# Optimization experiments

Measured on AMD Instinct MI355X. Metric: run time of the kernel, lower is better.

The kernel has to match this reference:

```python
import jax, jax.numpy as jnp
import numpy as np

N = 8192   # collocation points
H = 64     # hidden_dim (d_out of each KANLayer)
UH = 8     # unary_hidden_dim


def setup_inputs() -> dict:
    key = jax.random.key(0)
    ks = jax.random.split(key, 16)
    d = {}
    d["x"] = jax.random.normal(ks[0], (N, 1), dtype=jnp.float32)
    d["t"] = jax.random.normal(ks[1], (N, 1), dtype=jnp.float32)
    dims = [(2, H), (H, H), (H, H)]  # (d_in, d_out) per KANLayer
    idx = 2
    for l, (di, do) in enumerate(dims):
        d[f"W1_{l}"] = jax.random.normal(ks[idx], (do, di, UH), dtype=jnp.float32) * 0.5; idx += 1
        d[f"B1_{l}"] = jax.random.normal(ks[idx], (do, di, UH), dtype=jnp.float32) * 0.1; idx += 1
        d[f"W2_{l}"] = jax.random.normal(ks[idx], (do, di, UH), dtype=jnp.float32) * 0.5; idx += 1
        d[f"B2_{l}"] = jax.random.normal(ks[idx], (do, di), dtype=jnp.float32) * 0.1; idx += 1
    d["W_out"] = jax.random.normal(ks[14], (1, H), dtype=jnp.float32) * 0.1
    d["b_out"] = jnp.zeros((1,), dtype=jnp.float32)
    return d


def kan_layer(h, W1, B1, W2, B2):
    """Stacked KANLayer: y[n,j] = sum_i ( W2[j,i,:] . tanh(h[n,i]*W1[j,i,:] + B1[j,i,:]) + B2[j,i] ).
    h: (N, d_in); W1,B1,W2: (d_out, d_in, UH); B2: (d_out, d_in). Returns (N, d_out)."""
    hid = jnp.tanh(h[:, None, :, None] * W1[None] + B1[None])  # (N, d_out, d_in, UH)
    return jnp.einsum('ndih,dih->nd', hid, W2) + B2.sum(axis=1)


def reference(x, t, W1_0, B1_0, W2_0, B2_0, W1_1, B1_1, W2_1, B2_1,
              W1_2, B1_2, W2_2, B2_2, W_out, b_out):
    h = jnp.concatenate([x, t], axis=1)  # (N, 2)
    layers = [(W1_0, B1_0, W2_0, B2_0),
              (W1_1, B1_1, W2_1, B2_1),
              (W1_2, B1_2, W2_2, B2_2)]
    for W1, B1, W2, B2 in layers:
        h = jnp.tanh(kan_layer(h, W1, B1, W2, B2))
    u = h @ W_out.T + b_out  # (N, 1)
    return u
```

## Files before the change

kernel.cpp:

```cpp
#include <hip/hip_runtime.h>
#include <math.h>


#define C2L 2.88539008177792681472f
#define P_CHEB 20
#define M_SAMP 32

__device__ __forceinline__ float tanh_hw(float z) {
  float e = __builtin_amdgcn_exp2f(z * C2L);
  float r = __builtin_amdgcn_rcpf(1.0f + e);
  return fmaf(r, -2.0f, 1.0f);
}

__global__ __launch_bounds__(256) void kan_prep(
    const float* __restrict__ W1_1, const float* __restrict__ B1_1,
    const float* __restrict__ W2_1, const float* __restrict__ B2_1,
    const float* __restrict__ W1_2, const float* __restrict__ B1_2,
    const float* __restrict__ W2_2, const float* __restrict__ B2_2,
    float* __restrict__ G1, float* __restrict__ G2)
{
  const int g = blockIdx.x * 256 + threadIdx.x;
  const int k = g & 7;
  const int ji = (g >> 3) & 4095;
  const int layer = g >> 15;
  const float* __restrict__ W1 = layer ? W1_2 : W1_1;
  const float* __restrict__ B1 = layer ? B1_2 : B1_1;
  const float* __restrict__ W2 = layer ? W2_2 : W2_1;
  const float* __restrict__ B2 = layer ? B2_2 : B2_1;
  float* __restrict__ G = layer ? G2 : G1;

  const float w  = W1[ji * 8 + k];
  const float b  = B1[ji * 8 + k];
  const float w2 = W2[ji * 8 + k];

  float acc[P_CHEB];
#pragma unroll
  for (int p = 0; p < P_CHEB; ++p) acc[p] = 0.f;

  for (int m = 0; m < M_SAMP; ++m) {
    const float theta = ((float)m + 0.5f) * (3.14159265358979323846f / M_SAMP);
    const float c = cosf(theta);
    const float s = w2 * tanh_hw(fmaf(w, c, b));
    acc[0] += s;
    acc[1] = fmaf(s, c, acc[1]);
    const float c2 = c + c;
    float tp0 = 1.f, tp1 = c;
#pragma unroll
    for (int p = 2; p < P_CHEB; ++p) {
      const float t = fmaf(c2, tp1, -tp0);
      acc[p] = fmaf(s, t, acc[p]);
      tp0 = tp1; tp1 = t;
    }
  }
#pragma unroll
  for (int p = 0; p < P_CHEB; ++p) {
    float v = acc[p] * ((p == 0) ? (1.f / M_SAMP) : (2.f / M_SAMP));
    v += __shfl_xor(v, 1);
    v += __shfl_xor(v, 2);
    v += __shfl_xor(v, 4);
    acc[p] = v;
  }
  if (k == 0) {
    float* __restrict__ dst = G + ji * P_CHEB;
    acc[0] += B2[ji];
#pragma unroll
    for (int p = 0; p < P_CHEB; ++p) dst[p] = acc[p];
  }
}

__global__ __launch_bounds__(256) void kan_layer0(
    const float* __restrict__ x, const float* __restrict__ t,
    const float* __restrict__ W1, const float* __restrict__ B1,
    const float* __restrict__ W2, const float* __restrict__ B2,
    const float* __restrict__ bout,
    float* __restrict__ hA,
    float* __restrict__ out)
{
  const int tid  = threadIdx.x;
  const int lane = tid & 63;
  const int wave = __builtin_amdgcn_readfirstlane(tid >> 6);
  const int bx = blockIdx.x, by = blockIdx.y;
  const int flat = by * 128 + bx;
  if (flat < 32) out[flat * 256 + tid] = bout[0];

  const int n  = bx * 64 + lane;
  const int j0 = by * 16 + wave * 4;
  const float hx = x[n], ht = t[n];
#pragma unroll
  for (int jj = 0; jj < 4; ++jj) {
    const int j = j0 + jj;
    float a0 = B2[j * 2 + 0];
    float a1 = B2[j * 2 + 1];
#pragma unroll
    for (int k = 0; k < 8; ++k) {
      float z0 = fmaf(hx, W1[j * 16 + k], B1[j * 16 + k]);
      a0 = fmaf(W2[j * 16 + k], tanh_hw(z0), a0);
      float z1 = fmaf(ht, W1[j * 16 + 8 + k], B1[j * 16 + 8 + k]);
      a1 = fmaf(W2[j * 16 + 8 + k], tanh_hw(z1), a1);
    }
    hA[j * 8192 + n] = tanh_hw(a0 + a1);
  }
}

template <int HEAD>
__global__ __launch_bounds__(256, 4) void kan_cheb(
    const float* __restrict__ hin,
    const float* __restrict__ G,
    const float* __restrict__ Wout,
    float* __restrict__ outp)
{
  __shared__ float hs[64][64];
  __shared__ float red[4][64];
  const int tid  = threadIdx.x;
  const int lane = tid & 63;
  const int wave = __builtin_amdgcn_readfirstlane(tid >> 6);
  const int n    = blockIdx.x * 64 + lane;

#pragma unroll
  for (int r = 0; r < 16; ++r) {
    const int i = r * 4 + wave;
    hs[i][lane] = hin[i * 8192 + n];
  }
  __syncthreads();

  const int jA = blockIdx.y * 8 + wave * 2;
  const float4* __restrict__ gaq = (const float4*)(G + jA * (64 * P_CHEB));
  const float4* __restrict__ gbq = (const float4*)(G + (jA + 1) * (64 * P_CHEB));

  float aA0 = 0.f, aA1 = 0.f, aB0 = 0.f, aB1 = 0.f;
  for (int i = 0; i < 64; ++i) {
    const float h  = hs[i][lane];
    const float h2 = h + h;
    float ga[P_CHEB], gb[P_CHEB];
#pragma unroll
    for (int q = 0; q < P_CHEB / 4; ++q) {
      const float4 va = gaq[i * (P_CHEB / 4) + q];
      ga[4 * q + 0] = va.x; ga[4 * q + 1] = va.y; ga[4 * q + 2] = va.z; ga[4 * q + 3] = va.w;
      const float4 vb = gbq[i * (P_CHEB / 4) + q];
      gb[4 * q + 0] = vb.x; gb[4 * q + 1] = vb.y; gb[4 * q + 2] = vb.z; gb[4 * q + 3] = vb.w;
    }
    aA0 += ga[0];  aB0 += gb[0];
    aA1 = fmaf(ga[1], h, aA1);
    aB1 = fmaf(gb[1], h, aB1);
    float tp0 = 1.f, tp1 = h;
#pragma unroll
    for (int p = 2; p < P_CHEB; ++p) {
      const float tc = fmaf(h2, tp1, -tp0);
      if (p & 1) { aA1 = fmaf(ga[p], tc, aA1); aB1 = fmaf(gb[p], tc, aB1); }
      else       { aA0 = fmaf(ga[p], tc, aA0); aB0 = fmaf(gb[p], tc, aB0); }
      tp0 = tp1; tp1 = tc;
    }
  }
  const float yA = aA0 + aA1;
  const float yB = aB0 + aB1;

  if (HEAD) {
    red[wave][lane] = tanh_hw(yA) * Wout[jA] + tanh_hw(yB) * Wout[jA + 1];
    __syncthreads();
    if (wave == 0) {
      atomicAdd(&outp[n], (red[0][lane] + red[1][lane]) + (red[2][lane] + red[3][lane]));
    }
  } else {
    outp[jA * 8192 + n]       = tanh_hw(yA);
    outp[(jA + 1) * 8192 + n] = tanh_hw(yB);
  }
}

extern "C" void kernel_launch(void* const* d_in, const int* in_sizes, int n_in,
                              void* d_out, int out_size, void* d_ws, size_t ws_size,
                              hipStream_t stream) {
  const float* x    = (const float*)d_in[0];
  const float* t    = (const float*)d_in[1];
  const float* W1_0 = (const float*)d_in[2];
  const float* B1_0 = (const float*)d_in[3];
  const float* W2_0 = (const float*)d_in[4];
  const float* B2_0 = (const float*)d_in[5];
  const float* W1_1 = (const float*)d_in[6];
  const float* B1_1 = (const float*)d_in[7];
  const float* W2_1 = (const float*)d_in[8];
  const float* B2_1 = (const float*)d_in[9];
  const float* W1_2 = (const float*)d_in[10];
  const float* B1_2 = (const float*)d_in[11];
  const float* W2_2 = (const float*)d_in[12];
  const float* B2_2 = (const float*)d_in[13];
  const float* Wout = (const float*)d_in[14];
  const float* bout = (const float*)d_in[15];
  float* out = (float*)d_out;

  float* hA = (float*)d_ws;
  float* hB = hA + 64 * 8192;
  float* G1 = hB + 64 * 8192;
  float* G2 = G1 + 64 * 64 * P_CHEB;

  kan_prep<<<dim3(256), 256, 0, stream>>>(
      W1_1, B1_1, W2_1, B2_1, W1_2, B1_2, W2_2, B2_2, G1, G2);
  kan_layer0<<<dim3(128, 4), 256, 0, stream>>>(
      x, t, W1_0, B1_0, W2_0, B2_0, bout, hA, out);
  kan_cheb<0><<<dim3(128, 8), 256, 0, stream>>>(hA, G1, Wout, hB);
  kan_cheb<1><<<dim3(128, 8), 256, 0, stream>>>(hB, G2, Wout, out);
}
```

Measured before the change: 153.5 us.

## Lower Chebyshev degree, split input-sum across waves, and widen layer0 grid

```diff
diff --git a/kernel.cpp b/kernel.cpp
--- a/kernel.cpp
+++ b/kernel.cpp
@@ -3,7 +3,7 @@
 
 
 #define C2L 2.88539008177792681472f
-#define P_CHEB 20
+#define P_CHEB 16
 #define M_SAMP 32
 
 __device__ __forceinline__ float tanh_hw(float z) {
@@ -83,86 +83,141 @@
   const int flat = by * 128 + bx;
   if (flat < 32) out[flat * 256 + tid] = bout[0];
 
-  const int n  = bx * 64 + lane;
-  const int j0 = by * 16 + wave * 4;
+  const int n = bx * 64 + lane;
+  const int j = by * 4 + wave;
   const float hx = x[n], ht = t[n];
-#pragma unroll
-  for (int jj = 0; jj < 4; ++jj) {
-    const int j = j0 + jj;
-    float a0 = B2[j * 2 + 0];
-    float a1 = B2[j * 2 + 1];
-#pragma unroll
-    for (int k = 0; k < 8; ++k) {
-      float z0 = fmaf(hx, W1[j * 16 + k], B1[j * 16 + k]);
-      a0 = fmaf(W2[j * 16 + k], tanh_hw(z0), a0);
-      float z1 = fmaf(ht, W1[j * 16 + 8 + k], B1[j * 16 + 8 + k]);
-      a1 = fmaf(W2[j * 16 + 8 + k], tanh_hw(z1), a1);
-    }
-    hA[j * 8192 + n] = tanh_hw(a0 + a1);
-  }
+  float a0 = B2[j * 2 + 0];
+  float a1 = B2[j * 2 + 1];
+#pragma unroll
+  for (int k = 0; k < 8; ++k) {
+    float z0 = fmaf(hx, W1[j * 16 + k], B1[j * 16 + k]);
+    a0 = fmaf(W2[j * 16 + k], tanh_hw(z0), a0);
+    float z1 = fmaf(ht, W1[j * 16 + 8 + k], B1[j * 16 + 8 + k]);
+    a1 = fmaf(W2[j * 16 + 8 + k], tanh_hw(z1), a1);
+  }
+  hA[j * 8192 + n] = tanh_hw(a0 + a1);
 }
 
 template <int HEAD>
-__global__ __launch_bounds__(256, 4) void kan_cheb(
+__global__ __launch_bounds__(512, 8) void kan_cheb(
     const float* __restrict__ hin,
     const float* __restrict__ G,
     const float* __restrict__ Wout,
     float* __restrict__ outp)
 {
   __shared__ float hs[64][64];
-  __shared__ float red[4][64];
+  __shared__ float redA[8][64];
+  __shared__ float redB[8][64];
   const int tid  = threadIdx.x;
   const int lane = tid & 63;
   const int wave = __builtin_amdgcn_readfirstlane(tid >> 6);
   const int n    = blockIdx.x * 64 + lane;
 
 #pragma unroll
-  for (int r = 0; r < 16; ++r) {
-    const int i = r * 4 + wave;
+  for (int r = 0; r < 8; ++r) {
+    const int i = r * 8 + wave;
     hs[i][lane] = hin[i * 8192 + n];
   }
   __syncthreads();
 
-  const int jA = blockIdx.y * 8 + wave * 2;
+  const int jA = (blockIdx.y * 4 + (wave & 3)) * 2;
+  const int jB = jA + 1;
+  const int ihalf = wave >> 2;
   const float4* __restrict__ gaq = (const float4*)(G + jA * (64 * P_CHEB));
-  const float4* __restrict__ gbq = (const float4*)(G + (jA + 1) * (64 * P_CHEB));
+  const float4* __restrict__ gbq = (const float4*)(G + jB * (64 * P_CHEB));
 
   float aA0 = 0.f, aA1 = 0.f, aB0 = 0.f, aB1 = 0.f;
-  for (int i = 0; i < 64; ++i) {
+  const int i0 = ihalf * 32;
+  for (int i = i0; i < i0 + 32; ++i) {
     const float h  = hs[i][lane];
     const float h2 = h + h;
-    float ga[P_CHEB], gb[P_CHEB];
-#pragma unroll
-    for (int q = 0; q < P_CHEB / 4; ++q) {
-      const float4 va = gaq[i * (P_CHEB / 4) + q];
-      ga[4 * q + 0] = va.x; ga[4 * q + 1] = va.y; ga[4 * q + 2] = va.z; ga[4 * q + 3] = va.w;
-      const float4 vb = gbq[i * (P_CHEB / 4) + q];
-      gb[4 * q + 0] = vb.x; gb[4 * q + 1] = vb.y; gb[4 * q + 2] = vb.z; gb[4 * q + 3] = vb.w;
-    }
-    aA0 += ga[0];  aB0 += gb[0];
-    aA1 = fmaf(ga[1], h, aA1);
-    aB1 = fmaf(gb[1], h, aB1);
-    float tp0 = 1.f, tp1 = h;
-#pragma unroll
-    for (int p = 2; p < P_CHEB; ++p) {
-      const float tc = fmaf(h2, tp1, -tp0);
-      if (p & 1) { aA1 = fmaf(ga[p], tc, aA1); aB1 = fmaf(gb[p], tc, aB1); }
-      else       { aA0 = fmaf(ga[p], tc, aA0); aB0 = fmaf(gb[p], tc, aB0); }
-      tp0 = tp1; tp1 = tc;
-    }
-  }
-  const float yA = aA0 + aA1;
-  const float yB = aB0 + aB1;
+    const float t2  = fmaf(h2, h,  -1.f);
+    const float d2  = t2 + t2;
+    const float t3  = fmaf(h2, t2, -h);
+    const float t4  = fmaf(d2, t2, -1.f);
+    const float d3  = t3 + t3;
+    const float d4  = t4 + t4;
+    const float t5  = fmaf(d3, t2, -h);
+    const float t6  = fmaf(d3, t3, -1.f);
+    const float t7  = fmaf(d4, t3, -h);
+    const float t8  = fmaf(d4, t4, -1.f);
+    const float d5  = t5 + t5;
+    const float d6  = t6 + t6;
+    const float d7  = t7 + t7;
+    const float d8  = t8 + t8;
+    const float t9  = fmaf(d5, t4, -h);
+    const float t10 = fmaf(d5, t5, -1.f);
+    const float t11 = fmaf(d6, t5, -h);
+    const float t12 = fmaf(d6, t6, -1.f);
+    const float t13 = fmaf(d7, t6, -h);
+    const float t14 = fmaf(d7, t7, -1.f);
+    const float t15 = fmaf(d8, t7, -h);
+
+    const float4 va0 = gaq[i * 4 + 0];
+    const float4 va1 = gaq[i * 4 + 1];
+    const float4 va2 = gaq[i * 4 + 2];
+    const float4 va3 = gaq[i * 4 + 3];
+    aA0 += va0.x;
+    aA1 = fmaf(va0.y, h,   aA1);
+    aA0 = fmaf(va0.z, t2,  aA0);
+    aA1 = fmaf(va0.w, t3,  aA1);
+    aA0 = fmaf(va1.x, t4,  aA0);
+    aA1 = fmaf(va1.y, t5,  aA1);
+    aA0 = fmaf(va1.z, t6,  aA0);
+    aA1 = fmaf(va1.w, t7,  aA1);
+    aA0 = fmaf(va2.x, t8,  aA0);
+    aA1 = fmaf(va2.y, t9,  aA1);
+    aA0 = fmaf(va2.z, t10, aA0);
+    aA1 = fmaf(va2.w, t11, aA1);
+    aA0 = fmaf(va3.x, t12, aA0);
+    aA1 = fmaf(va3.y, t13, aA1);
+    aA0 = fmaf(va3.z, t14, aA0);
+    aA1 = fmaf(va3.w, t15, aA1);
+
+    const float4 vb0 = gbq[i * 4 + 0];
+    const float4 vb1 = gbq[i * 4 + 1];
+    const float4 vb2 = gbq[i * 4 + 2];
+    const float4 vb3 = gbq[i * 4 + 3];
+    aB0 += vb0.x;
+    aB1 = fmaf(vb0.y, h,   aB1);
+    aB0 = fmaf(vb0.z, t2,  aB0);
+    aB1 = fmaf(vb0.w, t3,  aB1);
+    aB0 = fmaf(vb1.x, t4,  aB0);
+    aB1 = fmaf(vb1.y, t5,  aB1);
+    aB0 = fmaf(vb1.z, t6,  aB0);
+    aB1 = fmaf(vb1.w, t7,  aB1);
+    aB0 = fmaf(vb2.x, t8,  aB0);
+    aB1 = fmaf(vb2.y, t9,  aB1);
+    aB0 = fmaf(vb2.z, t10, aB0);
+    aB1 = fmaf(vb2.w, t11, aB1);
+    aB0 = fmaf(vb3.x, t12, aB0);
+    aB1 = fmaf(vb3.y, t13, aB1);
+    aB0 = fmaf(vb3.z, t14, aB0);
+    aB1 = fmaf(vb3.w, t15, aB1);
+  }
+
+  redA[wave][lane] = aA0 + aA1;
+  redB[wave][lane] = aB0 + aB1;
+  __syncthreads();
 
   if (HEAD) {
-    red[wave][lane] = tanh_hw(yA) * Wout[jA] + tanh_hw(yB) * Wout[jA + 1];
+    if (wave < 4) {
+      const float yA = redA[wave][lane] + redA[wave + 4][lane];
+      const float yB = redB[wave][lane] + redB[wave + 4][lane];
+      redA[wave][lane] = tanh_hw(yA) * Wout[jA] + tanh_hw(yB) * Wout[jB];
+    }
     __syncthreads();
     if (wave == 0) {
-      atomicAdd(&outp[n], (red[0][lane] + red[1][lane]) + (red[2][lane] + red[3][lane]));
+      atomicAdd(&outp[n], (redA[0][lane] + redA[1][lane]) +
+                          (redA[2][lane] + redA[3][lane]));
     }
   } else {
-    outp[jA * 8192 + n]       = tanh_hw(yA);
-    outp[(jA + 1) * 8192 + n] = tanh_hw(yB);
+    if (wave < 4) {
+      const float yA = redA[wave][lane] + redA[wave + 4][lane];
+      const float yB = redB[wave][lane] + redB[wave + 4][lane];
+      outp[jA * 8192 + n] = tanh_hw(yA);
+      outp[jB * 8192 + n] = tanh_hw(yB);
+    }
   }
 }
 
@@ -194,8 +249,8 @@
 
   kan_prep<<<dim3(256), 256, 0, stream>>>(
       W1_1, B1_1, W2_1, B2_1, W1_2, B1_2, W2_2, B2_2, G1, G2);
-  kan_layer0<<<dim3(128, 4), 256, 0, stream>>>(
+  kan_layer0<<<dim3(128, 16), 256, 0, stream>>>(
       x, t, W1_0, B1_0, W2_0, B2_0, bout, hA, out);
-  kan_cheb<0><<<dim3(128, 8), 256, 0, stream>>>(hA, G1, Wout, hB);
-  kan_cheb<1><<<dim3(128, 8), 256, 0, stream>>>(hB, G2, Wout, out);
-}
+  kan_cheb<0><<<dim3(128, 8), 512, 0, stream>>>(hA, G1, Wout, hB);
+  kan_cheb<1><<<dim3(128, 8), 512, 0, stream>>>(hB, G2, Wout, out);
+}
```

Result: faster. 146.0 us (-4.9%).
